# Performance work log

Hardware: AMD Instinct MI355X
Metric: run time of the kernel (lower is better)

## Reference

```python
import jax, jax.numpy as jnp
import numpy as np

E, C, N, W_IN, W_OUT = 5, 2, 2048, 512, 256


def setup_inputs() -> dict:
    key = jax.random.key(0)
    ks = jax.random.split(key, 11)
    A = jax.random.uniform(ks[0], (E, N, N), dtype=jnp.float32)  # stacked edge-type adjacencies
    X = jax.random.normal(ks[1], (N, W_IN), dtype=jnp.float32)
    # GTConv weights (out_channels=C, in_channels=E), init std=0.01 as in torch
    gt_w0a = 0.01 * jax.random.normal(ks[2], (C, E), dtype=jnp.float32)
    gt_w0b = 0.01 * jax.random.normal(ks[3], (C, E), dtype=jnp.float32)
    gt_w1 = 0.01 * jax.random.normal(ks[4], (C, E), dtype=jnp.float32)
    gcn_w = jax.random.normal(ks[5], (W_IN, W_OUT), dtype=jnp.float32) / np.sqrt(W_IN)
    gcn_b = jnp.zeros((W_OUT,), dtype=jnp.float32)
    lin1_w = 0.02 * jax.random.normal(ks[6], (W_OUT, C * W_OUT), dtype=jnp.float32)
    lin1_b = jnp.zeros((W_OUT,), dtype=jnp.float32)
    lin2_w = 0.02 * jax.random.normal(ks[7], (W_OUT, W_OUT), dtype=jnp.float32)
    lin2_b = jnp.zeros((W_OUT,), dtype=jnp.float32)
    return {"A": A, "X": X, "gt_w0a": gt_w0a, "gt_w0b": gt_w0b, "gt_w1": gt_w1,
            "gcn_w": gcn_w, "gcn_b": gcn_b, "lin1_w": lin1_w, "lin1_b": lin1_b,
            "lin2_w": lin2_w, "lin2_b": lin2_b}


def _gtconv(w, A):
    # softmax over edge types, weighted sum of adjacencies == coalesce of scaled edge lists
    f = jax.nn.softmax(w, axis=1)  # (C, E)
    return jnp.einsum('ce,enm->cnm', f, A)  # (C, N, N)


def _normalize(H):
    # remove self loops, then divide each entry by its column (target) degree
    n = H.shape[-1]
    H = H * (1.0 - jnp.eye(n, dtype=H.dtype))
    deg = H.sum(axis=-2)                      # (C, N) column sums == scatter_add over col
    safe = jnp.where(deg != 0, deg, 1.0)
    dinv = jnp.where(deg != 0, 1.0 / safe, 0.0)
    return H * dinv[:, None, :]


def reference(A, X, gt_w0a, gt_w0b, gt_w1, gcn_w, gcn_b, lin1_w, lin1_b, lin2_w, lin2_b):
    # layer 0 (first=True): two GTConvs, per-channel spspmm == batched matmul
    Ha = _gtconv(gt_w0a, A)
    Hb = _gtconv(gt_w0b, A)
    H = _normalize(jnp.einsum('cij,cjk->cik', Ha, Hb))
    # layer 1 (first=False): H_ @ conv1(A)
    Hb2 = _gtconv(gt_w1, A)
    H = _normalize(jnp.einsum('cij,cjk->cik', H, Hb2))
    # GCNConv per channel: add self loops, symmetric deg^{-1/2} normalization, aggregate to col
    n = H.shape[-1]
    M = H + jnp.eye(n, dtype=H.dtype)         # (C, N, N)
    deg = M.sum(axis=-2)                      # (C, N)
    safe = jnp.where(deg > 0, deg, 1.0)
    dis = jnp.where(deg > 0, safe ** -0.5, 0.0)
    Ahat = dis[:, :, None] * M * dis[:, None, :]
    XW = X @ gcn_w                            # (N, W_OUT)
    out = jnp.einsum('crn,rf->cnf', Ahat, XW) + gcn_b  # out[c,n] = sum_r Ahat[c,r,n] XW[r]
    out = jax.nn.relu(out)                    # (C, N, W_OUT)
    Xcat = out.transpose(1, 0, 2).reshape(n, -1)       # concat channels along dim=1
    h = jax.nn.relu(Xcat @ lin1_w.T + lin1_b)
    return h @ lin2_w.T + lin2_b
```

## Files before the change

### kernel.cpp

```cpp
#include <hip/hip_runtime.h>
#include <cstdint>
#include <cstddef>

#define NN   2048
#define N2   (2048LL*2048LL)
#define CC   2
#define EE   5
#define WIN  512
#define WOUT 256

typedef __bf16 bf16_t;
typedef __attribute__((ext_vector_type(8))) __bf16 bf16x8;
typedef __attribute__((ext_vector_type(4))) __bf16 bf16x4;
typedef __attribute__((ext_vector_type(4))) float  f32x4;

#define AS1 __attribute__((address_space(1)))
#define AS3 __attribute__((address_space(3)))


__global__ __launch_bounds__(256, 2)
void k_combine(const float* __restrict__ A,
               const float* __restrict__ w0a, const float* __restrict__ w0b,
               const float* __restrict__ w1,
               bf16_t* __restrict__ Ha, bf16_t* __restrict__ HbT,
               bf16_t* __restrict__ Hb2T, float* __restrict__ part,
               const float* __restrict__ X, const float* __restrict__ l1w,
               const float* __restrict__ l2w, const float* __restrict__ gcnw,
               bf16_t* __restrict__ Xb, bf16_t* __restrict__ l1wb,
               bf16_t* __restrict__ l2wb, bf16_t* __restrict__ gwT) {
  __shared__ bf16_t tl[2][64][65];
  __shared__ float cs[2][4][64];
  int bid = blockIdx.x;
  int t = threadIdx.x;

  if (bid >= 1024) {
    int bid2 = bid - 1024;
    if (bid2 < 608) {
      int i = bid2 * 256 + t;
      const float* src; bf16_t* dst; int off;
      if (i < 131072)      { src = X;   dst = Xb;   off = i; }
      else if (i < 147456) { src = l1w; dst = l1wb; off = i - 131072; }
      else                 { src = l2w; dst = l2wb; off = i - 147456; }
      float4 a = ((const float4*)src)[off * 2];
      float4 b = ((const float4*)src)[off * 2 + 1];
      bf16x8 o;
      o[0] = (bf16_t)a.x; o[1] = (bf16_t)a.y; o[2] = (bf16_t)a.z; o[3] = (bf16_t)a.w;
      o[4] = (bf16_t)b.x; o[5] = (bf16_t)b.y; o[6] = (bf16_t)b.z; o[7] = (bf16_t)b.w;
      ((bf16x8*)dst)[off] = o;
    } else {
      int b2 = bid2 - 608;
      int m0 = (b2 & 7) * 64, n0 = (b2 >> 3) * 64;
      int tr = t >> 4, tc = (t & 15) << 2;
      bf16_t (*tile)[65] = (bf16_t (*)[65])&tl[0][0][0];
#pragma unroll
      for (int v = 0; v < 4; ++v) {
        int r = tr + v * 16;
        float4 d = *(const float4*)&gcnw[(long long)(m0 + r) * WOUT + n0 + tc];
        tile[r][tc + 0] = (bf16_t)d.x; tile[r][tc + 1] = (bf16_t)d.y;
        tile[r][tc + 2] = (bf16_t)d.z; tile[r][tc + 3] = (bf16_t)d.w;
      }
      __syncthreads();
#pragma unroll
      for (int v = 0; v < 4; ++v) {
        int r = tr + v * 16;
        bf16x4 o;
        o[0] = tile[tc + 0][r]; o[1] = tile[tc + 1][r];
        o[2] = tile[tc + 2][r]; o[3] = tile[tc + 3][r];
        *(bf16x4*)&gwT[(long long)(n0 + r) * WIN + m0 + tc] = o;
      }
    }
    return;
  }

  float f[3][2][5];
  {
    const float* wp[3] = {w0a, w0b, w1};
#pragma unroll
    for (int w = 0; w < 3; ++w)
#pragma unroll
      for (int c = 0; c < 2; ++c) {
        float x[5], m = -1e30f, s = 0.f;
#pragma unroll
        for (int e = 0; e < 5; ++e) { x[e] = wp[w][c * 5 + e]; m = fmaxf(m, x[e]); }
#pragma unroll
        for (int e = 0; e < 5; ++e) { x[e] = expf(x[e] - m); s += x[e]; }
#pragma unroll
        for (int e = 0; e < 5; ++e) f[w][c][e] = x[e] / s;
      }
  }
  int i0 = (bid >> 5) * 64, j0 = (bid & 31) * 64;
  int tr = t >> 4, tc = (t & 15) << 2;
  int lane = t & 63, wid = t >> 6;
  float cs0[4] = {0, 0, 0, 0}, cs1[4] = {0, 0, 0, 0};
  bf16x4 hb2a[4], hb2b[4];

  float4 q[5];
  {
    const float* b0 = A + (long long)(i0 + tr) * NN + j0 + tc;
#pragma unroll
    for (int e = 0; e < 5; ++e) q[e] = *(const float4*)(b0 + (long long)e * N2);
  }
#pragma unroll
  for (int v = 0; v < 4; ++v) {
    int lr = tr + v * 16;
    long long gi = i0 + lr;
    float av[5][4];
#pragma unroll
    for (int e = 0; e < 5; ++e) {
      av[e][0] = q[e].x; av[e][1] = q[e].y; av[e][2] = q[e].z; av[e][3] = q[e].w;
    }
    if (v < 3) {
      const float* bn = A + (gi + 16) * (long long)NN + j0 + tc;
#pragma unroll
      for (int e = 0; e < 5; ++e) q[e] = *(const float4*)(bn + (long long)e * N2);
    }
    bf16x4 ha0, ha1;
#pragma unroll
    for (int x = 0; x < 4; ++x) {
      float s0 = 0.f, s1 = 0.f, s2 = 0.f, s3 = 0.f, s4 = 0.f, s5 = 0.f;
#pragma unroll
      for (int e = 0; e < 5; ++e) {
        float u = av[e][x];
        s0 += f[0][0][e] * u; s1 += f[0][1][e] * u;
        s2 += f[1][0][e] * u; s3 += f[1][1][e] * u;
        s4 += f[2][0][e] * u; s5 += f[2][1][e] * u;
      }
      ha0[x] = (bf16_t)s0; cs0[x] += (float)ha0[x];
      ha1[x] = (bf16_t)s1; cs1[x] += (float)ha1[x];
      tl[0][lr][tc + x] = (bf16_t)s2; tl[1][lr][tc + x] = (bf16_t)s3;
      hb2a[v][x] = (bf16_t)s4; hb2b[v][x] = (bf16_t)s5;
    }
    *(bf16x4*)&Ha[0 * N2 + gi * NN + j0 + tc] = ha0;
    *(bf16x4*)&Ha[1 * N2 + gi * NN + j0 + tc] = ha1;
  }
#pragma unroll
  for (int x = 0; x < 4; ++x) {
    float a0 = cs0[x], a1 = cs1[x];
    a0 += __shfl_xor(a0, 16, 64); a0 += __shfl_xor(a0, 32, 64);
    a1 += __shfl_xor(a1, 16, 64); a1 += __shfl_xor(a1, 32, 64);
    if ((lane >> 4) == 0) {
      cs[0][wid][(lane & 15) * 4 + x] = a0;
      cs[1][wid][(lane & 15) * 4 + x] = a1;
    }
  }
  __syncthreads();

#pragma unroll
  for (int v = 0; v < 4; ++v) {
    int lr = tr + v * 16;
#pragma unroll
    for (int ch = 0; ch < 2; ++ch) {
      bf16x4 o;
      o[0] = tl[ch][tc + 0][lr]; o[1] = tl[ch][tc + 1][lr];
      o[2] = tl[ch][tc + 2][lr]; o[3] = tl[ch][tc + 3][lr];
      *(bf16x4*)&HbT[(long long)ch * N2 + (long long)(j0 + lr) * NN + i0 + tc] = o;
    }
  }
  if (t < 128) {
    int ch = t >> 6, col = t & 63;
    float s = cs[ch][0][col] + cs[ch][1][col] + cs[ch][2][col] + cs[ch][3][col];
    part[((long long)ch * 32 + (bid >> 5)) * NN + j0 + col] = s;
  }
  __syncthreads();

#pragma unroll
  for (int v = 0; v < 4; ++v) {
    int lr = tr + v * 16;
#pragma unroll
    for (int x = 0; x < 4; ++x) {
      tl[0][lr][tc + x] = hb2a[v][x];
      tl[1][lr][tc + x] = hb2b[v][x];
    }
  }
  __syncthreads();

#pragma unroll
  for (int v = 0; v < 4; ++v) {
    int lr = tr + v * 16;
#pragma unroll
    for (int ch = 0; ch < 2; ++ch) {
      bf16x4 o;
      o[0] = tl[ch][tc + 0][lr]; o[1] = tl[ch][tc + 1][lr];
      o[2] = tl[ch][tc + 2][lr]; o[3] = tl[ch][tc + 3][lr];
      *(bf16x4*)&Hb2T[(long long)ch * N2 + (long long)(j0 + lr) * NN + i0 + tc] = o;
    }
  }
}

__global__ void k_s_finish(const float* __restrict__ part, float* __restrict__ s) {
  int idx = blockIdx.x * 256 + threadIdx.x;
  int c = idx >> 11, k = idx & 2047;
  float acc = 0.f;
#pragma unroll
  for (int ib = 0; ib < 32; ++ib) acc += part[((long long)c * 32 + ib) * NN + k];
  s[idx] = acc;
}

template<bool EMIT_DIS>
__global__ void k_deg(const float* __restrict__ svec, const bf16_t* __restrict__ Arows,
                      const bf16_t* __restrict__ BT,
                      float* __restrict__ out1, float* __restrict__ out2,
                      float* __restrict__ out3) {
  int c = blockIdx.y;
  int j = blockIdx.x * 4 + (threadIdx.x >> 6);
  int lane = threadIdx.x & 63;
  const bf16_t* a = Arows + (long long)c * N2 + (long long)j * NN;
  const bf16_t* b = BT + (long long)c * N2 + (long long)j * NN;
  const float* s = svec + c * NN;
  float acc_s = 0.f, acc_a = 0.f;
#pragma unroll
  for (int it = 0; it < 4; ++it) {
    int k0 = (lane + it * 64) * 8;
    bf16x8 av = *(const bf16x8*)(a + k0);
    bf16x8 bv = *(const bf16x8*)(b + k0);
    float4 s0 = *(const float4*)(s + k0);
    float4 s1 = *(const float4*)(s + k0 + 4);
    float sv[8] = {s0.x, s0.y, s0.z, s0.w, s1.x, s1.y, s1.z, s1.w};
#pragma unroll
    for (int x = 0; x < 8; ++x) {
      float bx = (float)bv[x];
      acc_s += sv[x] * bx;
      acc_a += (float)av[x] * bx;
    }
  }
#pragma unroll
  for (int o = 32; o > 0; o >>= 1) {
    acc_s += __shfl_xor(acc_s, o, 64);
    acc_a += __shfl_xor(acc_a, o, 64);
  }
  if (lane == 0) {
    float deg = acc_s - acc_a;
    bool nz = (deg != 0.f);
    if (!EMIT_DIS) {
      out1[c * NN + j] = nz ? 1.f / deg : 0.f;
      out2[c * NN + j] = nz ? 1.f : 0.f;
    } else {
      float dis = nz ? 0.70710678118654752f : 1.f;
      out1[c * NN + j] = nz ? dis / deg : 0.f;
      out2[c * NN + j] = dis;
      out3[c * NN + j] = acc_a;
    }
  }
}


__global__ __launch_bounds__(256)
void k_gemmL(const bf16_t* __restrict__ A, const bf16_t* __restrict__ B,
             bf16_t* __restrict__ Hn, bf16_t* __restrict__ HnT,
             const float* __restrict__ dinv) {
  __shared__ __align__(16) char smem[65536];
  bf16_t* As = (bf16_t*)smem;
  bf16_t* Bs = (bf16_t*)(smem + 32768);
  bf16_t* tile = (bf16_t*)smem;

  int cz = blockIdx.z;
  const bf16_t* Ab = A + cz * N2 + (long long)blockIdx.x * 128 * NN;
  const bf16_t* Bb = B + cz * N2 + (long long)blockIdx.y * 128 * NN;

  int t = threadIdx.x, wid = t >> 6, lane = t & 63;
  int wr = wid >> 1, wc = wid & 1;
  f32x4 acc[4][4] = {};
  int frow = lane & 15;
  int fk_sw = (((lane >> 4) ^ ((frow >> 1) & 3)) << 3);
  int srow = t >> 2;
  int scol_sw = (((t & 3) ^ ((t >> 3) & 3)) << 3);

  auto STAGE = [&](int TT, int BUF) {
#pragma unroll
    for (int s = 0; s < 2; ++s) {
      long long kko = (long long)TT * 64 + s * 32 + scol_sw;
      const bf16_t* ga0 = Ab + (long long)srow * NN + kko;
      const bf16_t* gb0 = Bb + (long long)srow * NN + kko;
      char* la = smem + BUF * 16384 + s * 8192 + wid * 1024;
      char* lb = smem + 32768 + BUF * 16384 + s * 8192 + wid * 1024;
      __builtin_amdgcn_global_load_lds((AS1 void*)ga0, (AS3 void*)la, 16, 0, 0);
      __builtin_amdgcn_global_load_lds((AS1 void*)(ga0 + 64LL * NN), (AS3 void*)(la + 4096), 16, 0, 0);
      __builtin_amdgcn_global_load_lds((AS1 void*)gb0, (AS3 void*)lb, 16, 0, 0);
      __builtin_amdgcn_global_load_lds((AS1 void*)(gb0 + 64LL * NN), (AS3 void*)(lb + 4096), 16, 0, 0);
    }
  };
  auto COMPUTE = [&](int BUF) {
#pragma unroll
    for (int ks = 0; ks < 2; ++ks) {
      bf16x8 af[4], bfr[4];
#pragma unroll
      for (int m = 0; m < 4; ++m)
        af[m] = *(const bf16x8*)&As[BUF * 8192 + ks * 4096 + (wr * 64 + m * 16 + frow) * 32 + fk_sw];
#pragma unroll
      for (int n = 0; n < 4; ++n)
        bfr[n] = *(const bf16x8*)&Bs[BUF * 8192 + ks * 4096 + (wc * 64 + n * 16 + frow) * 32 + fk_sw];
      __builtin_amdgcn_s_setprio(1);
#pragma unroll
      for (int m = 0; m < 4; ++m)
#pragma unroll
        for (int n = 0; n < 4; ++n)
          acc[m][n] = __builtin_amdgcn_mfma_f32_16x16x32_bf16(af[m], bfr[n], acc[m][n], 0, 0, 0);
      __builtin_amdgcn_s_setprio(0);
    }
  };

  const int nt = 32;
  STAGE(0, 0); STAGE(1, 1);
  for (int tt = 0; tt < nt; ++tt) {
    if (tt < nt - 1) asm volatile("s_waitcnt vmcnt(8)" ::: "memory");
    else             asm volatile("s_waitcnt vmcnt(0)" ::: "memory");
    __builtin_amdgcn_s_barrier();
    __builtin_amdgcn_sched_barrier(0);
    COMPUTE(tt & 1);
    __builtin_amdgcn_s_barrier();
    if (tt + 2 < nt) STAGE(tt + 2, tt & 1);
  }
  __builtin_amdgcn_sched_barrier(0);

  int rl0 = wr * 64 + ((lane >> 4) << 2);
  int cl0 = wc * 64 + (lane & 15);
  int r0 = blockIdx.x * 128 + rl0;
  int c0 = blockIdx.y * 128 + cl0;

  bf16_t* Cb = Hn + cz * N2;
  bf16_t* Ct = HnT + cz * N2;
  float dj[4];
#pragma unroll
  for (int n = 0; n < 4; ++n) dj[n] = dinv[cz * NN + c0 + n * 16];
#pragma unroll
  for (int m = 0; m < 4; ++m)
#pragma unroll
    for (int n = 0; n < 4; ++n)
#pragma unroll
      for (int j = 0; j < 4; ++j) {
        int r = r0 + m * 16 + j, col = c0 + n * 16;
        float v = (r == col) ? 0.f : acc[m][n][j] * dj[n];
        Cb[(long long)r * NN + col] = (bf16_t)v;
        tile[(rl0 + m * 16 + j) * 130 + cl0 + n * 16] = (bf16_t)v;
      }
  __syncthreads();
  int nl = t >> 5, rl = (t & 31) * 4;
#pragma unroll
  for (int vv = 0; vv < 16; ++vv) {
    int n_l = nl + vv * 8;
    bf16x4 o;
    o[0] = tile[(rl + 0) * 130 + n_l]; o[1] = tile[(rl + 1) * 130 + n_l];
    o[2] = tile[(rl + 2) * 130 + n_l]; o[3] = tile[(rl + 3) * 130 + n_l];
    *(bf16x4*)&Ct[(long long)(blockIdx.y * 128 + n_l) * NN + blockIdx.x * 128 + rl] = o;
  }
}


enum { EP_BRELU = 3, EP_BF32 = 4, EP_BF16O = 7, EP_XWDT = 8, EP_GCN = 9 };

template<int EP>
__global__ __launch_bounds__(256)
void k_gemm(const bf16_t* __restrict__ A, const bf16_t* __restrict__ B,
            void* __restrict__ Cv,
            const float* __restrict__ aux1, const float* __restrict__ aux2,
            bf16_t* __restrict__ aux3, const float* __restrict__ aux4,
            int N, int K, int lda, int ldb,
            long long zA, long long zB, long long zC) {
  __shared__ __align__(16) char smem[36864];
  bf16_t* As = (bf16_t*)smem;
  bf16_t* Bs = (bf16_t*)(smem + 24576);
  bf16_t* tile = (bf16_t*)smem;

  int cz = blockIdx.z;
  const bf16_t* Ab = A + cz * zA + (long long)blockIdx.x * 128 * lda;
  const bf16_t* Bb = B + cz * zB + (long long)blockIdx.y * 64 * ldb;

  int t = threadIdx.x, wid = t >> 6, lane = t & 63;
  int wr = wid >> 1, wc = wid & 1;
  f32x4 acc[4][2] = {};
  int frow = lane & 15;
  int fk_sw = (((lane >> 4) ^ ((frow >> 1) & 3)) << 3);
  int srow = t >> 2;
  int scol_sw = (((t & 3) ^ ((t >> 3) & 3)) << 3);
  int nt = K >> 5;

  auto STAGE = [&](int TT, int BUF) {
    long long kko = (long long)TT * 32 + scol_sw;
    const bf16_t* ga0 = Ab + (long long)srow * lda + kko;
    const bf16_t* ga1 = Ab + (long long)(64 + srow) * lda + kko;
    const bf16_t* gb0 = Bb + (long long)srow * ldb + kko;
    char* la = smem + BUF * 8192 + wid * 1024;
    char* lb = smem + 24576 + BUF * 4096 + wid * 1024;
    __builtin_amdgcn_global_load_lds((AS1 void*)ga0, (AS3 void*)la, 16, 0, 0);
    __builtin_amdgcn_global_load_lds((AS1 void*)ga1, (AS3 void*)(la + 4096), 16, 0, 0);
    __builtin_amdgcn_global_load_lds((AS1 void*)gb0, (AS3 void*)lb, 16, 0, 0);
  };
  auto COMPUTE = [&](int BUF) {
    bf16x8 af[4], bfr[2];
#pragma unroll
    for (int m = 0; m < 4; ++m)
      af[m] = *(const bf16x8*)&As[BUF * 4096 + (wr * 64 + m * 16 + frow) * 32 + fk_sw];
#pragma unroll
    for (int n = 0; n < 2; ++n)
      bfr[n] = *(const bf16x8*)&Bs[BUF * 2048 + (wc * 32 + n * 16 + frow) * 32 + fk_sw];
#pragma unroll
    for (int m = 0; m < 4; ++m)
#pragma unroll
      for (int n = 0; n < 2; ++n)
        acc[m][n] = __builtin_amdgcn_mfma_f32_16x16x32_bf16(af[m], bfr[n], acc[m][n], 0, 0, 0);
  };

  STAGE(0, 0); STAGE(1, 1); STAGE(2, 2);
  int slot = 0;
  for (int tt = 0; tt < nt; ++tt) {
    int rem = nt - 1 - tt;
    if (rem >= 2)      asm volatile("s_waitcnt vmcnt(6)" ::: "memory");
    else if (rem == 1) asm volatile("s_waitcnt vmcnt(3)" ::: "memory");
    else               asm volatile("s_waitcnt vmcnt(0)" ::: "memory");
    __builtin_amdgcn_s_barrier();
    __builtin_amdgcn_sched_barrier(0);
    COMPUTE(slot);
    __builtin_amdgcn_s_barrier();
    if (tt + 3 < nt) STAGE(tt + 3, slot);
    slot = (slot == 2) ? 0 : slot + 1;
  }
  __builtin_amdgcn_sched_barrier(0);

  int rl0 = wr * 64 + ((lane >> 4) << 2);
  int cl0 = wc * 32 + (lane & 15);
  int r0 = blockIdx.x * 128 + rl0;
  int c0 = blockIdx.y * 64 + cl0;

  if constexpr (EP == EP_BF16O) {
    bf16_t* Cb = (bf16_t*)Cv + cz * zC;
#pragma unroll
    for (int m = 0; m < 4; ++m)
#pragma unroll
      for (int n = 0; n < 2; ++n)
#pragma unroll
        for (int j = 0; j < 4; ++j)
          Cb[(long long)(r0 + m * 16 + j) * N + c0 + n * 16] = (bf16_t)acc[m][n][j];
  } else if constexpr (EP == EP_XWDT) {
    float* Cb = (float*)Cv;
#pragma unroll
    for (int m = 0; m < 4; ++m)
#pragma unroll
      for (int n = 0; n < 2; ++n)
#pragma unroll
        for (int j = 0; j < 4; ++j) {
          float v = acc[m][n][j];
          Cb[(long long)(r0 + m * 16 + j) * N + c0 + n * 16] = v;
          tile[(rl0 + m * 16 + j) * 65 + cl0 + n * 16] = (bf16_t)v;
        }
    __syncthreads();
    int nl = t >> 5, rl = (t & 31) * 4;
#pragma unroll
    for (int vv = 0; vv < 8; ++vv) {
      int n_l = nl + vv * 8;
      bf16x4 v4;
      v4[0] = tile[(rl + 0) * 65 + n_l]; v4[1] = tile[(rl + 1) * 65 + n_l];
      v4[2] = tile[(rl + 2) * 65 + n_l]; v4[3] = tile[(rl + 3) * 65 + n_l];
      int i0 = blockIdx.x * 128 + rl;
      long long row = (long long)(blockIdx.y * 64 + n_l) * NN + i0;
#pragma unroll
      for (int c = 0; c < 2; ++c) {
        float4 dv = *(const float4*)&aux2[c * NN + i0];
        bf16x4 o;
        o[0] = (bf16_t)((float)v4[0] * dv.x); o[1] = (bf16_t)((float)v4[1] * dv.y);
        o[2] = (bf16_t)((float)v4[2] * dv.z); o[3] = (bf16_t)((float)v4[3] * dv.w);
        *(bf16x4*)&aux3[(long long)c * WOUT * NN + row] = o;
      }
    }
  } else if constexpr (EP == EP_GCN) {
    bf16_t* Cb = (bf16_t*)Cv;
    const float* XWp = aux1;
    const float* csp = aux2 + cz * NN;
    const float* dnp = aux2 + CC * NN + cz * NN;
    const float* mdp = aux2 + 2 * CC * NN + cz * NN;
    float bj[2];
#pragma unroll
    for (int n = 0; n < 2; ++n) bj[n] = aux4[c0 + n * 16];
#pragma unroll
    for (int m = 0; m < 4; ++m)
#pragma unroll
      for (int j = 0; j < 4; ++j) {
        int r = r0 + m * 16 + j;
        float csv = csp[r], dnv = dnp[r], mdv = mdp[r];
        float mdd = mdv * dnv, d2 = dnv * dnv;
#pragma unroll
        for (int n = 0; n < 2; ++n) {
          float xw = XWp[(long long)r * WOUT + c0 + n * 16];
          float v = fmaxf(csv * (acc[m][n][j] - mdd * xw) + d2 * xw + bj[n], 0.f);
          Cb[(long long)r * (CC * WOUT) + cz * WOUT + c0 + n * 16] = (bf16_t)v;
        }
      }
  } else if constexpr (EP == EP_BRELU) {
    bf16_t* Cb = (bf16_t*)Cv;
    float bj[2];
#pragma unroll
    for (int n = 0; n < 2; ++n) bj[n] = aux1[c0 + n * 16];
#pragma unroll
    for (int m = 0; m < 4; ++m)
#pragma unroll
      for (int n = 0; n < 2; ++n)
#pragma unroll
        for (int j = 0; j < 4; ++j)
          Cb[(long long)(r0 + m * 16 + j) * N + c0 + n * 16] =
              (bf16_t)fmaxf(acc[m][n][j] + bj[n], 0.f);
  } else {
    float* Cb = (float*)Cv;
    float bj[2];
#pragma unroll
    for (int n = 0; n < 2; ++n) bj[n] = aux1[c0 + n * 16];
#pragma unroll
    for (int m = 0; m < 4; ++m)
#pragma unroll
      for (int n = 0; n < 2; ++n)
#pragma unroll
        for (int j = 0; j < 4; ++j)
          Cb[(long long)(r0 + m * 16 + j) * N + c0 + n * 16] = acc[m][n][j] + bj[n];
  }
}


extern "C" void kernel_launch(void* const* d_in, const int* in_sizes, int n_in,
                              void* d_out, int out_size, void* d_ws, size_t ws_size,
                              hipStream_t stream) {
  const float* A    = (const float*)d_in[0];
  const float* X    = (const float*)d_in[1];
  const float* w0a  = (const float*)d_in[2];
  const float* w0b  = (const float*)d_in[3];
  const float* w1   = (const float*)d_in[4];
  const float* gcnw = (const float*)d_in[5];
  const float* gcnb = (const float*)d_in[6];
  const float* l1w  = (const float*)d_in[7];
  const float* l1b  = (const float*)d_in[8];
  const float* l2w  = (const float*)d_in[9];
  const float* l2b  = (const float*)d_in[10];
  float* out = (float*)d_out;

  char* p = (char*)d_ws;
  auto carve = [&](size_t bytes) -> char* {
    char* r = p; p += (bytes + 255) & ~(size_t)255; return r;
  };
  float*  svec  = (float*)carve((size_t)CC * NN * 4);
  float*  dinv1 = (float*)carve((size_t)CC * NN * 4);
  float*  m1    = (float*)carve((size_t)CC * NN * 4);
  float*  scal  = (float*)carve((size_t)3 * CC * NN * 4);
  float*  part  = (float*)carve((size_t)CC * 32 * NN * 4);
  bf16_t* S1    = (bf16_t*)carve((size_t)CC * N2 * 2);
  bf16_t* HbT   = (bf16_t*)carve((size_t)CC * N2 * 2);
  bf16_t* Hb2T  = (bf16_t*)carve((size_t)CC * N2 * 2);
  bf16_t* Hn    = (bf16_t*)carve((size_t)CC * N2 * 2);
  bf16_t* HnT   = (bf16_t*)carve((size_t)CC * N2 * 2);
  bf16_t* Xb    = (bf16_t*)carve((size_t)NN * WIN * 2);
  bf16_t* gwT   = (bf16_t*)carve((size_t)WOUT * WIN * 2);
  bf16_t* l1wb  = (bf16_t*)carve((size_t)WOUT * CC * WOUT * 2);
  bf16_t* l2wb  = (bf16_t*)carve((size_t)WOUT * WOUT * 2);
  float*  XW    = (float*)carve((size_t)NN * WOUT * 4);
  bf16_t* Xcat  = (bf16_t*)carve((size_t)NN * CC * WOUT * 2);
  bf16_t* hb    = (bf16_t*)carve((size_t)NN * WOUT * 2);

  bf16_t* Ha = S1;
  bf16_t* XWdT = (bf16_t*)((char*)S1);
  bf16_t* Yt   = (bf16_t*)((char*)S1 + (2LL << 20));
  float*  disv = scal + CC * NN;

  k_combine<<<1664, 256, 0, stream>>>(A, w0a, w0b, w1, Ha, HbT, Hb2T, part,
                                      X, l1w, l2w, gcnw, Xb, l1wb, l2wb, gwT);
  k_s_finish<<<16, 256, 0, stream>>>(part, svec);

  k_deg<false><<<dim3(512, 2), 256, 0, stream>>>(svec, Ha, HbT, dinv1, m1, nullptr);
  k_gemmL<<<dim3(16, 16, 2), 256, 0, stream>>>(Ha, HbT, Hn, HnT, dinv1);

  k_deg<true><<<dim3(512, 2), 256, 0, stream>>>(m1, Hn, Hb2T,
                                                scal, scal + CC * NN, scal + 2 * CC * NN);

  k_gemm<EP_XWDT><<<dim3(16, 4, 1), 256, 0, stream>>>(
      Xb, gwT, XW, nullptr, disv, XWdT, nullptr, WOUT, WIN, WIN, WIN, 0, 0, 0);
  k_gemm<EP_BF16O><<<dim3(2, 32, 2), 256, 0, stream>>>(
      XWdT, HnT, Yt, nullptr, nullptr, nullptr, nullptr, NN, NN, NN, NN,
      (long long)WOUT * NN, N2, (long long)WOUT * NN);
  k_gemm<EP_GCN><<<dim3(16, 4, 2), 256, 0, stream>>>(
      Hb2T, Yt, Xcat, XW, scal, nullptr, gcnb, WOUT, NN, NN, NN,
      N2, (long long)WOUT * NN, 0);

  k_gemm<EP_BRELU><<<dim3(16, 4, 1), 256, 0, stream>>>(
      Xcat, l1wb, hb, l1b, nullptr, nullptr, nullptr, WOUT, CC * WOUT, CC * WOUT, CC * WOUT, 0, 0, 0);
  k_gemm<EP_BF32><<<dim3(16, 4, 1), 256, 0, stream>>>(
      hb, l2wb, out, l2b, nullptr, nullptr, nullptr, WOUT, WOUT, WOUT, WOUT, 0, 0, 0);
}
```

Before: 142.4 us.

## Fuse second degree reduction into first GEMM epilogue, drop row-major Hn write

After: 141.2 us. Within noise of the previous version (-0.8%).

```diff
diff --git a/kernel.cpp b/kernel.cpp
--- a/kernel.cpp
+++ b/kernel.cpp
@@ -196,11 +196,9 @@
   s[idx] = acc;
 }
 
-template<bool EMIT_DIS>
-__global__ void k_deg(const float* __restrict__ svec, const bf16_t* __restrict__ Arows,
-                      const bf16_t* __restrict__ BT,
-                      float* __restrict__ out1, float* __restrict__ out2,
-                      float* __restrict__ out3) {
+__global__ void k_deg1(const float* __restrict__ svec, const bf16_t* __restrict__ Arows,
+                       const bf16_t* __restrict__ BT,
+                       float* __restrict__ out1, float* __restrict__ out2) {
   int c = blockIdx.y;
   int j = blockIdx.x * 4 + (threadIdx.x >> 6);
   int lane = threadIdx.x & 63;
@@ -231,27 +229,40 @@
   if (lane == 0) {
     float deg = acc_s - acc_a;
     bool nz = (deg != 0.f);
-    if (!EMIT_DIS) {
-      out1[c * NN + j] = nz ? 1.f / deg : 0.f;
-      out2[c * NN + j] = nz ? 1.f : 0.f;
-    } else {
-      float dis = nz ? 0.70710678118654752f : 1.f;
-      out1[c * NN + j] = nz ? dis / deg : 0.f;
-      out2[c * NN + j] = dis;
-      out3[c * NN + j] = acc_a;
-    }
-  }
+    out1[c * NN + j] = nz ? 1.f / deg : 0.f;
+    out2[c * NN + j] = nz ? 1.f : 0.f;
+  }
+}
+
+__global__ void k_deg2_finish(const float* __restrict__ pd, const float* __restrict__ pm,
+                              float* __restrict__ scal) {
+  int idx = blockIdx.x * 256 + threadIdx.x;
+  int c = idx >> 11, r = idx & 2047;
+  float deg = 0.f, md = 0.f;
+#pragma unroll
+  for (int by = 0; by < 16; ++by) {
+    deg += pd[((long long)by * CC + c) * NN + r];
+    md  += pm[((long long)by * CC + c) * NN + r];
+  }
+  bool nz = (deg != 0.f);
+  float dis = nz ? 0.70710678118654752f : 1.f;
+  scal[c * NN + r] = nz ? dis / deg : 0.f;
+  scal[CC * NN + c * NN + r] = dis;
+  scal[2 * CC * NN + c * NN + r] = md;
 }
 
 
 __global__ __launch_bounds__(256)
 void k_gemmL(const bf16_t* __restrict__ A, const bf16_t* __restrict__ B,
-             bf16_t* __restrict__ Hn, bf16_t* __restrict__ HnT,
-             const float* __restrict__ dinv) {
+             bf16_t* __restrict__ HnT, const float* __restrict__ dinv,
+             const float* __restrict__ m1, const bf16_t* __restrict__ Hb2T,
+             float* __restrict__ pd, float* __restrict__ pm) {
   __shared__ __align__(16) char smem[65536];
   bf16_t* As = (bf16_t*)smem;
   bf16_t* Bs = (bf16_t*)(smem + 32768);
   bf16_t* tile = (bf16_t*)smem;
+  float* sbd = (float*)(smem + 34816);
+  float* sbm = (float*)(smem + 34816 + 1024);
 
   int cz = blockIdx.z;
   const bf16_t* Ab = A + cz * N2 + (long long)blockIdx.x * 128 * NN;
@@ -317,11 +328,63 @@
   int r0 = blockIdx.x * 128 + rl0;
   int c0 = blockIdx.y * 128 + cl0;
 
-  bf16_t* Cb = Hn + cz * N2;
   bf16_t* Ct = HnT + cz * N2;
-  float dj[4];
-#pragma unroll
-  for (int n = 0; n < 4; ++n) dj[n] = dinv[cz * NN + c0 + n * 16];
+  const bf16_t* Hb2 = Hb2T + cz * N2;
+  float dj[4], m1v[4];
+#pragma unroll
+  for (int n = 0; n < 4; ++n) {
+    dj[n] = dinv[cz * NN + c0 + n * 16];
+    m1v[n] = m1[cz * NN + c0 + n * 16];
+  }
+
+  float pdeg[4][4], pmd[4][4];
+#pragma unroll
+  for (int m = 0; m < 4; ++m)
+#pragma unroll
+    for (int j = 0; j < 4; ++j) {
+      int r = r0 + m * 16 + j;
+      const bf16_t* hrow = Hb2 + (long long)r * NN;
+      float ad = 0.f, am = 0.f;
+#pragma unroll
+      for (int n = 0; n < 4; ++n) {
+        int col = c0 + n * 16;
+        float hv = (r == col) ? 0.f : (float)(bf16_t)(acc[m][n][j] * dj[n]);
+        float hb = (float)hrow[col];
+        am += hv * hb;
+        ad += (m1v[n] - hv) * hb;
+      }
+      pdeg[m][j] = ad; pmd[m][j] = am;
+    }
+#pragma unroll
+  for (int m = 0; m < 4; ++m)
+#pragma unroll
+    for (int j = 0; j < 4; ++j) {
+#pragma unroll
+      for (int msk = 1; msk <= 8; msk <<= 1) {
+        pdeg[m][j] += __shfl_xor(pdeg[m][j], msk, 64);
+        pmd[m][j]  += __shfl_xor(pmd[m][j], msk, 64);
+      }
+    }
+  if ((lane & 15) == 0) {
+#pragma unroll
+    for (int m = 0; m < 4; ++m)
+#pragma unroll
+      for (int j = 0; j < 4; ++j) {
+        int lrw = m * 16 + ((lane >> 4) << 2) + j;
+        sbd[wid * 64 + lrw] = pdeg[m][j];
+        sbm[wid * 64 + lrw] = pmd[m][j];
+      }
+  }
+  __syncthreads();
+  if (t < 128) {
+    int wrof = t >> 6, lr6 = t & 63;
+    float dsum = sbd[(wrof * 2 + 0) * 64 + lr6] + sbd[(wrof * 2 + 1) * 64 + lr6];
+    float msum = sbm[(wrof * 2 + 0) * 64 + lr6] + sbm[(wrof * 2 + 1) * 64 + lr6];
+    long long r = (long long)blockIdx.x * 128 + t;
+    pd[((long long)blockIdx.y * CC + cz) * NN + r] = dsum;
+    pm[((long long)blockIdx.y * CC + cz) * NN + r] = msum;
+  }
+
 #pragma unroll
   for (int m = 0; m < 4; ++m)
 #pragma unroll
@@ -330,7 +393,6 @@
       for (int j = 0; j < 4; ++j) {
         int r = r0 + m * 16 + j, col = c0 + n * 16;
         float v = (r == col) ? 0.f : acc[m][n][j] * dj[n];
-        Cb[(long long)r * NN + col] = (bf16_t)v;
         tile[(rl0 + m * 16 + j) * 130 + cl0 + n * 16] = (bf16_t)v;
       }
   __syncthreads();
@@ -538,10 +600,11 @@
   float*  m1    = (float*)carve((size_t)CC * NN * 4);
   float*  scal  = (float*)carve((size_t)3 * CC * NN * 4);
   float*  part  = (float*)carve((size_t)CC * 32 * NN * 4);
+  float*  pd    = (float*)carve((size_t)16 * CC * NN * 4);
+  float*  pmg   = (float*)carve((size_t)16 * CC * NN * 4);
   bf16_t* S1    = (bf16_t*)carve((size_t)CC * N2 * 2);
   bf16_t* HbT   = (bf16_t*)carve((size_t)CC * N2 * 2);
   bf16_t* Hb2T  = (bf16_t*)carve((size_t)CC * N2 * 2);
-  bf16_t* Hn    = (bf16_t*)carve((size_t)CC * N2 * 2);
   bf16_t* HnT   = (bf16_t*)carve((size_t)CC * N2 * 2);
   bf16_t* Xb    = (bf16_t*)carve((size_t)NN * WIN * 2);
   bf16_t* gwT   = (bf16_t*)carve((size_t)WOUT * WIN * 2);
@@ -560,11 +623,9 @@
                                       X, l1w, l2w, gcnw, Xb, l1wb, l2wb, gwT);
   k_s_finish<<<16, 256, 0, stream>>>(part, svec);
 
-  k_deg<false><<<dim3(512, 2), 256, 0, stream>>>(svec, Ha, HbT, dinv1, m1, nullptr);
-  k_gemmL<<<dim3(16, 16, 2), 256, 0, stream>>>(Ha, HbT, Hn, HnT, dinv1);
-
-  k_deg<true><<<dim3(512, 2), 256, 0, stream>>>(m1, Hn, Hb2T,
-                                                scal, scal + CC * NN, scal + 2 * CC * NN);
+  k_deg1<<<dim3(512, 2), 256, 0, stream>>>(svec, Ha, HbT, dinv1, m1);
+  k_gemmL<<<dim3(16, 16, 2), 256, 0, stream>>>(Ha, HbT, HnT, dinv1, m1, Hb2T, pd, pmg);
+  k_deg2_finish<<<16, 256, 0, stream>>>(pd, pmg, scal);
 
   k_gemm<EP_XWDT><<<dim3(16, 4, 1), 256, 0, stream>>>(
       Xb, gwT, XW, nullptr, disv, XWdT, nullptr, WOUT, WIN, WIN, WIN, 0, 0, 0);
```
